# Optimization experiments

Hardware: AMD Instinct MI355X
Metric: run time of the kernel (lower is better)

## Reference

```python
import jax, jax.numpy as jnp
import numpy as np

N, E, M = 100000, 3200000, 1000000  # nodes, message edges, scored move edges
DIN, H = 128, 64


def setup_inputs() -> dict:
    key = jax.random.key(0)
    ks = jax.random.split(key, 20)
    rn = lambda k, shape, s=0.05: (jax.random.normal(k, shape, jnp.float32) * s)
    return {
        "x": jax.random.normal(ks[0], (N, DIN), jnp.float32),
        "edge_index": jax.random.randint(ks[1], (2, E), 0, N, jnp.int64),
        "move_edge_index": jax.random.randint(ks[2], (2, M), 0, N, jnp.int64),
        "lin1_w": rn(ks[3], (DIN, H)), "lin1_b": jnp.zeros((H,), jnp.float32),
        "lin2_w": rn(ks[4], (H, H)), "lin2_b": jnp.zeros((H,), jnp.float32),
        "conv1_wl": rn(ks[5], (H, H)), "conv1_bl": jnp.zeros((H,), jnp.float32),
        "conv1_wr": rn(ks[6], (H, H)),
        "conv2_wl": rn(ks[7], (H, H)), "conv2_bl": jnp.zeros((H,), jnp.float32),
        "conv2_wr": rn(ks[8], (H, H)),
        "mlp_w1": rn(ks[9], (2 * H, H)), "mlp_b1": jnp.zeros((H,), jnp.float32),
        "mlp_w2": rn(ks[10], (H, 1)), "mlp_b2": jnp.zeros((1,), jnp.float32),
    }


def reference(x, edge_index, move_edge_index,
              lin1_w, lin1_b, lin2_w, lin2_b,
              conv1_wl, conv1_bl, conv1_wr,
              conv2_wl, conv2_bl, conv2_wr,
              mlp_w1, mlp_b1, mlp_w2, mlp_b2):
    n = x.shape[0]
    src, dst = edge_index[0], edge_index[1]
    # mean-aggregation degrees (PyG SAGEConv default aggr='mean'; isolated nodes -> 0)
    deg = jax.ops.segment_sum(jnp.ones(src.shape, x.dtype), dst, num_segments=n)
    inv_deg = (jnp.where(deg > 0, 1.0 / jnp.maximum(deg, 1.0), 0.0))[:, None]

    def sage(h, wl, bl, wr):
        # out = W_l @ mean_j h_j + b_l + W_r @ h_i
        agg = jax.ops.segment_sum(h[src], dst, num_segments=n) * inv_deg
        return agg @ wl + bl + h @ wr

    h = jax.nn.relu(x @ lin1_w + lin1_b)
    h = jax.nn.relu(sage(h, conv1_wl, conv1_bl, conv1_wr))
    h = jax.nn.relu(h @ lin2_w + lin2_b)
    h = jax.nn.relu(sage(h, conv2_wl, conv2_bl, conv2_wr))

    # edge scoring: gather src/dst embeddings, concat, 2-layer MLP, tanh
    cat = jnp.concatenate([h[move_edge_index[0]], h[move_edge_index[1]]], axis=1)  # [M, 2H]
    logits = (jax.nn.relu(cat @ mlp_w1 + mlp_b1) @ mlp_w2 + mlp_b2).reshape(-1)
    return jnp.tanh(logits)
```

## Files before the change

### kernel.cpp

```cpp
#include <hip/hip_runtime.h>
#include <math.h>

#define MAXB 512
#define PART_BS 1024
#define NBLK_MAX 248
#define CAPB 96

typedef _Float16 f16;
typedef __attribute__((ext_vector_type(2))) _Float16 f16x2;
typedef __attribute__((ext_vector_type(4))) _Float16 f16x4;
typedef __attribute__((ext_vector_type(8))) _Float16 f16x8;
typedef __attribute__((ext_vector_type(4))) float f32x4;

static __device__ __forceinline__ unsigned short f2h(float f) {
    f16 h = (f16)f; return *(unsigned short*)&h;
}

__global__ __launch_bounds__(PART_BS) void k_part(const int* __restrict__ src,
                                                  const int* __restrict__ dst,
                                                  unsigned* __restrict__ bb,
                                                  int* __restrict__ cnt,
                                                  int E, int shift, int pcap,
                                                  int nblk, int nb) {
    __shared__ int h[MAXB];
    const int blk = blockIdx.x;
    const int b0 = blk * pcap;
    const int e1 = min(b0 + pcap, E);
    for (int i = threadIdx.x; i < MAXB; i += PART_BS) h[i] = 0;
    __syncthreads();
    const unsigned mask = (1u << shift) - 1u;
    for (int pos = b0 + (int)threadIdx.x * 8; pos < e1; pos += PART_BS * 8) {
        if (pos + 8 <= e1) {
            int4 d0 = *(const int4*)(dst + pos), d1 = *(const int4*)(dst + pos + 4);
            int4 s0 = *(const int4*)(src + pos), s1 = *(const int4*)(src + pos + 4);
            int dd[8] = {d0.x, d0.y, d0.z, d0.w, d1.x, d1.y, d1.z, d1.w};
            int ss[8] = {s0.x, s0.y, s0.z, s0.w, s1.x, s1.y, s1.z, s1.w};
#pragma unroll
            for (int k = 0; k < 8; ++k) {
                int b = dd[k] >> shift;
                int r = atomicAdd(&h[b], 1);
                if (r < CAPB)
                    bb[((size_t)b * nblk + blk) * CAPB + r] =
                        ((unsigned)ss[k] << shift) | ((unsigned)dd[k] & mask);
            }
        } else {
            for (int k = 0; pos + k < e1; ++k) {
                int d = dst[pos + k];
                int b = d >> shift;
                int r = atomicAdd(&h[b], 1);
                if (r < CAPB)
                    bb[((size_t)b * nblk + blk) * CAPB + r] =
                        ((unsigned)src[pos + k] << shift) | ((unsigned)d & mask);
            }
        }
    }
    __syncthreads();
    for (int i = threadIdx.x; i < nb; i += PART_BS)
        cnt[(size_t)i * nblk + blk] = min(h[i], CAPB);
}

__global__ __launch_bounds__(512) void k_bfill(const unsigned* __restrict__ bb,
                                               const int* __restrict__ cnt,
                                               int* __restrict__ row_st,
                                               int* __restrict__ row_en,
                                               float* __restrict__ inv_deg,
                                               int* __restrict__ csr,
                                               int N, int shift, int CAP, int nblk) {
    __shared__ int deg[512], cur[512], s[512];
    __shared__ int scnt[NBLK_MAX];
    int b = blockIdx.x;
    int t = threadIdx.x;
    int lo = b << shift;
    int hi = min(N, (b + 1) << shift);
    int nn = hi - lo;
    unsigned off = (unsigned)b * CAP;
    unsigned mask = (1u << shift) - 1u;
    const unsigned* seg = bb + (size_t)b * nblk * CAPB;

    for (int i = t; i < nblk; i += 512) scnt[i] = cnt[(size_t)b * nblk + i];
    deg[t] = 0;
    __syncthreads();
    const int tot = nblk * CAPB;
    for (int i = t; i < tot; i += 512) {
        int si = i / CAPB;
        int r = i - si * CAPB;
        if (r < scnt[si])
            atomicAdd(&deg[seg[i] & mask], 1);
    }
    __syncthreads();
    int d = deg[t];
    int pd = (d + 31) & ~31;
    s[t] = pd;
    __syncthreads();
    for (int o = 1; o < 512; o <<= 1) {
        int u = (t >= o) ? s[t - o] : 0;
        __syncthreads();
        s[t] += u;
        __syncthreads();
    }
    int excl = min(s[t] - pd, CAP);
    int pe = min(excl + pd, CAP);
    cur[t] = excl;
    if (t < nn) {
        row_st[lo + t] = (int)off + excl;
        row_en[lo + t] = (int)off + pe;
        inv_deg[lo + t] = d > 0 ? 1.0f / (float)d : 0.0f;
        for (int j = excl + d; j < pe; ++j) csr[off + j] = N;
    }
    __syncthreads();
    for (int i = t; i < tot; i += 512) {
        int si = i / CAPB;
        int r = i - si * CAPB;
        if (r < scnt[si]) {
            unsigned w = seg[i];
            int dl = (int)(w & mask);
            int pos = atomicAdd(&cur[dl], 1);
            if (pos < CAP) csr[off + pos] = (int)(w >> shift);
        }
    }
}

__global__ __launch_bounds__(256) void k_prep(
    const float* __restrict__ lin1_w, const float* __restrict__ c1_wl,
    const float* __restrict__ c1_wr, const float* __restrict__ lin2_w,
    const float* __restrict__ c2_wl, const float* __restrict__ c2_wr,
    const float* __restrict__ mlp_w1, const float* __restrict__ mlp_w2,
    unsigned short* __restrict__ Wt) {
    int i = blockIdx.x * 256 + threadIdx.x;
    for (; i < 36928; i += gridDim.x * 256) {
        float v;
        if (i < 8192)       { int j = i;         int n = j >> 7, k = j & 127; v = lin1_w[k * 64 + n]; }
        else if (i < 16384) { int j = i - 8192;  int n = j >> 7, k = j & 127;
                              v = (k < 64) ? c1_wl[k * 64 + n] : c1_wr[(k - 64) * 64 + n]; }
        else if (i < 20480) { int j = i - 16384; int n = j >> 6, k = j & 63;  v = lin2_w[k * 64 + n]; }
        else if (i < 28672) { int j = i - 20480; int n = j >> 7, k = j & 127;
                              v = (k < 64) ? c2_wl[k * 64 + n] : c2_wr[(k - 64) * 64 + n]; }
        else if (i < 32768) { int j = i - 28672; int n = j >> 6, k = j & 63;  v = mlp_w1[k * 64 + n]; }
        else if (i < 36864) { int j = i - 32768; int n = j >> 6, k = j & 63;  v = mlp_w1[(k + 64) * 64 + n]; }
        else                { v = mlp_w2[i - 36864]; }
        Wt[i] = f2h(v);
    }
}

__global__ __launch_bounds__(256) void k_gather_h(
    const _Float16* __restrict__ hh, const int* __restrict__ csr,
    const int* __restrict__ row_st, const int* __restrict__ row_en,
    const float* __restrict__ inv_deg, _Float16* __restrict__ out, int n) {
    int node = (blockIdx.x * 256 + (int)threadIdx.x) >> 6;
    if (node >= n) return;
    int lane = threadIdx.x & 63;
    int g = lane >> 3, sub = lane & 7;
    int base = row_st[node], end = row_en[node];
    float a[8] = {0.f, 0.f, 0.f, 0.f, 0.f, 0.f, 0.f, 0.f};
#if __has_builtin(__builtin_amdgcn_fdot2)
    const f16x2 one2 = {(f16)1.f, (f16)1.f};
#endif
    for (; base + 64 <= end; base += 64) {
        int4 sA = *(const int4*)&csr[base + 4 * g];
        int4 sB = *(const int4*)&csr[base + 32 + 4 * g];
        int sidx[8] = {sA.x, sA.y, sA.z, sA.w, sB.x, sB.y, sB.z, sB.w};
        f16x8 u[8];
#pragma unroll
        for (int t = 0; t < 8; ++t)
            u[t] = *(const f16x8*)(hh + (((unsigned)sidx[t] << 6) + ((unsigned)sub << 3)));
#if __has_builtin(__builtin_amdgcn_fdot2)
#pragma unroll
        for (int t = 0; t < 8; t += 2)
#pragma unroll
            for (int j = 0; j < 8; ++j) {
                f16x2 v = {u[t][j], u[t + 1][j]};
                a[j] = __builtin_amdgcn_fdot2(v, one2, a[j], false);
            }
#else
#pragma unroll
        for (int t = 0; t < 8; ++t)
#pragma unroll
            for (int j = 0; j < 8; ++j) a[j] += (float)u[t][j];
#endif
    }
    if (base < end) {
        int4 sA = *(const int4*)&csr[base + 4 * g];
        int sidx[4] = {sA.x, sA.y, sA.z, sA.w};
        f16x8 u[4];
#pragma unroll
        for (int t = 0; t < 4; ++t)
            u[t] = *(const f16x8*)(hh + (((unsigned)sidx[t] << 6) + ((unsigned)sub << 3)));
#if __has_builtin(__builtin_amdgcn_fdot2)
#pragma unroll
        for (int t = 0; t < 4; t += 2)
#pragma unroll
            for (int j = 0; j < 8; ++j) {
                f16x2 v = {u[t][j], u[t + 1][j]};
                a[j] = __builtin_amdgcn_fdot2(v, one2, a[j], false);
            }
#else
#pragma unroll
        for (int t = 0; t < 4; ++t)
#pragma unroll
            for (int j = 0; j < 8; ++j) a[j] += (float)u[t][j];
#endif
    }
#pragma unroll
    for (int j = 0; j < 8; ++j) {
        a[j] += __shfl_xor(a[j], 8, 64);
        a[j] += __shfl_xor(a[j], 16, 64);
        a[j] += __shfl_xor(a[j], 32, 64);
    }
    if (g == 0) {
        float idv = inv_deg[node];
        f16x8 o;
#pragma unroll
        for (int j = 0; j < 8; ++j) o[j] = (f16)(a[j] * idv);
        *(f16x8*)(out + (((unsigned)node << 6) + ((unsigned)sub << 3))) = o;
    }
}

__global__ __launch_bounds__(256) void k_mm1(
    const float* __restrict__ x, const unsigned short* __restrict__ Wtg,
    const float* __restrict__ bias, unsigned short* __restrict__ outh, int n) {
    __shared__ alignas(16) unsigned short sW[64 * 136];
    const int tid = threadIdx.x;
    const int row0 = blockIdx.x * 64;
    if (blockIdx.x == 0 && tid < 8)
        ((uint4*)(outh + (size_t)n * 64))[tid] = (uint4){0, 0, 0, 0};
    for (int i = tid; i < 64 * 16; i += 256) {
        int nn = i >> 4, c = i & 15;
        *(uint4*)&sW[(nn * 17 + c) * 8] = *(const uint4*)&Wtg[i * 8];
    }
    __syncthreads();
    const int lane = tid & 63, w = tid >> 6;
    const int m = lane & 15, q = lane >> 4;
    const int gr = min(row0 + 16 * w + m, n - 1);
    const float* ar = x + (size_t)gr * 128;
    f32x4 acc[4];
#pragma unroll
    for (int c = 0; c < 4; ++c) acc[c] = (f32x4){0.f, 0.f, 0.f, 0.f};
#pragma unroll
    for (int kk = 0; kk < 4; ++kk) {
        float4 a0 = *(const float4*)(ar + kk * 32 + q * 8);
        float4 a1 = *(const float4*)(ar + kk * 32 + q * 8 + 4);
        f16x8 af;
        af[0] = (f16)a0.x; af[1] = (f16)a0.y; af[2] = (f16)a0.z; af[3] = (f16)a0.w;
        af[4] = (f16)a1.x; af[5] = (f16)a1.y; af[6] = (f16)a1.z; af[7] = (f16)a1.w;
#pragma unroll
        for (int c = 0; c < 4; ++c) {
            f16x8 bf = *(const f16x8*)&sW[((16 * c + m) * 17 + (kk * 4 + q)) * 8];
            acc[c] = __builtin_amdgcn_mfma_f32_16x16x32_f16(af, bf, acc[c], 0, 0, 0);
        }
    }
#pragma unroll
    for (int c = 0; c < 4; ++c) {
        int col = 16 * c + m;
        float bv = bias[col];
#pragma unroll
        for (int i = 0; i < 4; ++i) {
            int r = row0 + 16 * w + q * 4 + i;
            if (r < n) outh[(size_t)r * 64 + col] = f2h(fmaxf(acc[c][i] + bv, 0.f));
        }
    }
}

__global__ __launch_bounds__(256) void k_mm23(
    const unsigned short* __restrict__ aggH, const unsigned short* __restrict__ h1,
    const unsigned short* __restrict__ Wcg, const float* __restrict__ bl,
    const unsigned short* __restrict__ Wl2g, const float* __restrict__ b2,
    unsigned short* __restrict__ outh, int n) {
    __shared__ alignas(16) unsigned short sm[64 * 72 + 64 * 136];
    unsigned short* hA = sm;
    unsigned short* sW = sm + 64 * 72;
    const int tid = threadIdx.x;
    const int row0 = blockIdx.x * 64;
    for (int i = tid; i < 64 * 16; i += 256) {
        int nn = i >> 4, c = i & 15;
        *(uint4*)&sW[(nn * 17 + c) * 8] = *(const uint4*)&Wcg[i * 8];
    }
    __syncthreads();
    const int lane = tid & 63, w = tid >> 6;
    const int m = lane & 15, q = lane >> 4;
    const int gr = min(row0 + 16 * w + m, n - 1);
    f32x4 acc[4];
#pragma unroll
    for (int c = 0; c < 4; ++c) acc[c] = (f32x4){0.f, 0.f, 0.f, 0.f};
#pragma unroll
    for (int kk = 0; kk < 4; ++kk) {
        const unsigned short* ap = (kk < 2)
            ? (aggH + (size_t)gr * 64 + kk * 32 + q * 8)
            : (h1 + (size_t)gr * 64 + (kk - 2) * 32 + q * 8);
        f16x8 af = *(const f16x8*)ap;
#pragma unroll
        for (int c = 0; c < 4; ++c) {
            f16x8 bf = *(const f16x8*)&sW[((16 * c + m) * 17 + (kk * 4 + q)) * 8];
            acc[c] = __builtin_amdgcn_mfma_f32_16x16x32_f16(af, bf, acc[c], 0, 0, 0);
        }
    }
#pragma unroll
    for (int c = 0; c < 4; ++c) {
        int col = 16 * c + m;
        float bv = bl[col];
#pragma unroll
        for (int i = 0; i < 4; ++i)
            hA[(16 * w + q * 4 + i) * 72 + col] = f2h(fmaxf(acc[c][i] + bv, 0.f));
    }
    __syncthreads();
    for (int i = tid; i < 64 * 8; i += 256) {
        int nn = i >> 3, c = i & 7;
        *(uint4*)&sW[(nn * 9 + c) * 8] = *(const uint4*)&Wl2g[i * 8];
    }
    __syncthreads();
    f32x4 acc2[4];
#pragma unroll
    for (int c = 0; c < 4; ++c) acc2[c] = (f32x4){0.f, 0.f, 0.f, 0.f};
#pragma unroll
    for (int kk = 0; kk < 2; ++kk) {
        f16x8 af = *(const f16x8*)&hA[(16 * w + m) * 72 + kk * 32 + q * 8];
#pragma unroll
        for (int c = 0; c < 4; ++c) {
            f16x8 bf = *(const f16x8*)&sW[((16 * c + m) * 9 + (kk * 4 + q)) * 8];
            acc2[c] = __builtin_amdgcn_mfma_f32_16x16x32_f16(af, bf, acc2[c], 0, 0, 0);
        }
    }
#pragma unroll
    for (int c = 0; c < 4; ++c) {
        int col = 16 * c + m;
        float bv = b2[col];
#pragma unroll
        for (int i = 0; i < 4; ++i) {
            int r = row0 + 16 * w + q * 4 + i;
            if (r < n) outh[(size_t)r * 64 + col] = f2h(fmaxf(acc2[c][i] + bv, 0.f));
        }
    }
}

__global__ __launch_bounds__(256) void k_mm456(
    const unsigned short* __restrict__ aggH, const unsigned short* __restrict__ h3,
    const unsigned short* __restrict__ Wcg, const float* __restrict__ bl,
    const unsigned short* __restrict__ Wpg, const unsigned short* __restrict__ Wqg,
    const float* __restrict__ b1, unsigned short* __restrict__ Ph,
    unsigned short* __restrict__ Qh, int n) {
    __shared__ alignas(16) unsigned short sm[64 * 72 + 2 * 64 * 72];
    unsigned short* hA = sm;
    unsigned short* sW = sm + 64 * 72;
    const int tid = threadIdx.x;
    const int row0 = blockIdx.x * 64;
    for (int i = tid; i < 64 * 16; i += 256) {
        int nn = i >> 4, c = i & 15;
        *(uint4*)&sW[(nn * 17 + c) * 8] = *(const uint4*)&Wcg[i * 8];
    }
    __syncthreads();
    const int lane = tid & 63, w = tid >> 6;
    const int m = lane & 15, q = lane >> 4;
    const int gr = min(row0 + 16 * w + m, n - 1);
    f32x4 acc[4];
#pragma unroll
    for (int c = 0; c < 4; ++c) acc[c] = (f32x4){0.f, 0.f, 0.f, 0.f};
#pragma unroll
    for (int kk = 0; kk < 4; ++kk) {
        const unsigned short* ap = (kk < 2)
            ? (aggH + (size_t)gr * 64 + kk * 32 + q * 8)
            : (h3 + (size_t)gr * 64 + (kk - 2) * 32 + q * 8);
        f16x8 af = *(const f16x8*)ap;
#pragma unroll
        for (int c = 0; c < 4; ++c) {
            f16x8 bf = *(const f16x8*)&sW[((16 * c + m) * 17 + (kk * 4 + q)) * 8];
            acc[c] = __builtin_amdgcn_mfma_f32_16x16x32_f16(af, bf, acc[c], 0, 0, 0);
        }
    }
#pragma unroll
    for (int c = 0; c < 4; ++c) {
        int col = 16 * c + m;
        float bv = bl[col];
#pragma unroll
        for (int i = 0; i < 4; ++i)
            hA[(16 * w + q * 4 + i) * 72 + col] = f2h(fmaxf(acc[c][i] + bv, 0.f));
    }
    __syncthreads();
    for (int i = tid; i < 64 * 8; i += 256) {
        int nn = i >> 3, c = i & 7;
        *(uint4*)&sW[(nn * 9 + c) * 8] = *(const uint4*)&Wpg[i * 8];
        *(uint4*)&sW[4608 + (nn * 9 + c) * 8] = *(const uint4*)&Wqg[i * 8];
    }
    __syncthreads();
    f32x4 accP[4], accQ[4];
#pragma unroll
    for (int c = 0; c < 4; ++c) {
        accP[c] = (f32x4){0.f, 0.f, 0.f, 0.f};
        accQ[c] = (f32x4){0.f, 0.f, 0.f, 0.f};
    }
#pragma unroll
    for (int kk = 0; kk < 2; ++kk) {
        f16x8 af = *(const f16x8*)&hA[(16 * w + m) * 72 + kk * 32 + q * 8];
#pragma unroll
        for (int c = 0; c < 4; ++c) {
            f16x8 bp = *(const f16x8*)&sW[((16 * c + m) * 9 + (kk * 4 + q)) * 8];
            f16x8 bq = *(const f16x8*)&sW[4608 + ((16 * c + m) * 9 + (kk * 4 + q)) * 8];
            accP[c] = __builtin_amdgcn_mfma_f32_16x16x32_f16(af, bp, accP[c], 0, 0, 0);
            accQ[c] = __builtin_amdgcn_mfma_f32_16x16x32_f16(af, bq, accQ[c], 0, 0, 0);
        }
    }
#pragma unroll
    for (int c = 0; c < 4; ++c) {
        int col = 16 * c + m;
        float bv = b1[col];
#pragma unroll
        for (int i = 0; i < 4; ++i) {
            int r = row0 + 16 * w + q * 4 + i;
            if (r < n) {
                Ph[(size_t)r * 64 + col] = f2h(accP[c][i] + bv);
                Qh[(size_t)r * 64 + col] = f2h(accQ[c][i]);
            }
        }
    }
}

__global__ __launch_bounds__(256) void k_score_h(
    const _Float16* __restrict__ P, const _Float16* __restrict__ Q,
    const int* __restrict__ msrc, const int* __restrict__ mdst,
    const _Float16* __restrict__ w2h, const float* __restrict__ b2,
    float* __restrict__ out, int M) {
    int gid = blockIdx.x * 256 + threadIdx.x;
    int e = gid >> 3;
    if (e >= M) return;
    int l = gid & 7;
    int s = msrc[e], d = mdst[e];
    f16x8 p = *(const f16x8*)(P + (((unsigned)s << 6) + ((unsigned)l << 3)));
    f16x8 q = *(const f16x8*)(Q + (((unsigned)d << 6) + ((unsigned)l << 3)));
    f16x8 w = *(const f16x8*)(w2h + ((unsigned)l << 3));
    f16x8 u = p + q;
    f16x8 z = {(f16)0, (f16)0, (f16)0, (f16)0, (f16)0, (f16)0, (f16)0, (f16)0};
    u = __builtin_elementwise_max(u, z);
    float partial;
#if __has_builtin(__builtin_amdgcn_fdot2)
    f16x2 u01 = {u[0], u[1]}, u23 = {u[2], u[3]}, u45 = {u[4], u[5]}, u67 = {u[6], u[7]};
    f16x2 w01 = {w[0], w[1]}, w23 = {w[2], w[3]}, w45 = {w[4], w[5]}, w67 = {w[6], w[7]};
    partial = __builtin_amdgcn_fdot2(u01, w01,
              __builtin_amdgcn_fdot2(u23, w23,
              __builtin_amdgcn_fdot2(u45, w45,
              __builtin_amdgcn_fdot2(u67, w67, 0.f, false), false), false), false);
#else
    partial = 0.f;
#pragma unroll
    for (int i = 0; i < 8; ++i) partial += (float)u[i] * (float)w[i];
#endif
    partial += __shfl_xor(partial, 1, 8);
    partial += __shfl_xor(partial, 2, 8);
    partial += __shfl_xor(partial, 4, 8);
    if (l == 0) {
        float xx = partial + b2[0];
        float t = __expf(2.f * xx);
        out[e] = (t - 1.f) / (t + 1.f);
    }
}

extern "C" void kernel_launch(void* const* d_in, const int* in_sizes, int n_in,
                              void* d_out, int out_size, void* d_ws, size_t ws_size,
                              hipStream_t stream) {
    const float* x      = (const float*)d_in[0];
    const int*   ei     = (const int*)d_in[1];
    const int*   mei    = (const int*)d_in[2];
    const float* lin1_w = (const float*)d_in[3];
    const float* lin1_b = (const float*)d_in[4];
    const float* lin2_w = (const float*)d_in[5];
    const float* lin2_b = (const float*)d_in[6];
    const float* c1_wl  = (const float*)d_in[7];
    const float* c1_bl  = (const float*)d_in[8];
    const float* c1_wr  = (const float*)d_in[9];
    const float* c2_wl  = (const float*)d_in[10];
    const float* c2_bl  = (const float*)d_in[11];
    const float* c2_wr  = (const float*)d_in[12];
    const float* mlp_w1 = (const float*)d_in[13];
    const float* mlp_b1 = (const float*)d_in[14];
    const float* mlp_w2 = (const float*)d_in[15];
    const float* mlp_b2 = (const float*)d_in[16];

    const int N = in_sizes[0] / 128;
    const int E = in_sizes[1] / 2;
    const int M = in_sizes[2] / 2;
    const int* src  = ei;
    const int* dstE = ei + E;
    const int* msrc = mei;
    const int* mdst = mei + M;

    int shift = 8;
    while ((((N - 1) >> shift) + 1) > MAXB) ++shift;
    const int nbuckets = ((N - 1) >> shift) + 1;
    long long avg = (((long long)E << shift) / N) + 1;
    int CAP = (int)((2 * avg + 2047) & ~1023LL);

    const size_t N64 = (size_t)N * 64;
    const size_t aliasBytes = (3 * N64 + 64) * 2;
    int nblk = NBLK_MAX;
    while (nblk > 1 && (size_t)nblk * nbuckets * CAPB * 4 > aliasBytes) --nblk;
    int pcap = (((E + nblk - 1) / nblk) + 7) & ~7;
    nblk = (E + pcap - 1) / pcap;

    unsigned short* Hh   = (unsigned short*)d_ws;
    unsigned short* aggH = Hh + N64 + 64;
    unsigned short* Qh   = aggH + N64;
    float* inv_deg = (float*)(Qh + N64);
    int*   row_st  = (int*)(inv_deg + N);
    int*   row_en  = row_st + N;
    int*   cnt     = row_en + N;
    unsigned short* Wt = (unsigned short*)(cnt + (size_t)nbuckets * NBLK_MAX);
    int*   csr     = (int*)(Wt + 36928 + 32);
    unsigned* bb   = (unsigned*)Hh;
    float* outf = (float*)d_out;

    const int nbN = (N + 63) / 64;
    const int nbM = (int)(((long long)M * 8 + 255) / 256);
    const int nbG = (int)(((long long)N * 64 + 255) / 256);

    k_prep<<<64, 256, 0, stream>>>(lin1_w, c1_wl, c1_wr, lin2_w, c2_wl, c2_wr,
                                   mlp_w1, mlp_w2, Wt);
    k_part<<<nblk, PART_BS, 0, stream>>>(src, dstE, bb, cnt, E, shift, pcap,
                                         nblk, nbuckets);
    k_bfill<<<nbuckets, 512, 0, stream>>>(bb, cnt, row_st, row_en,
                                          inv_deg, csr, N, shift, CAP, nblk);

    k_mm1<<<nbN, 256, 0, stream>>>(x, Wt + 0, lin1_b, Hh, N);

    k_gather_h<<<nbG, 256, 0, stream>>>((const _Float16*)Hh, csr, row_st, row_en,
                                        inv_deg, (_Float16*)aggH, N);
    k_mm23<<<nbN, 256, 0, stream>>>(aggH, Hh, Wt + 8192, c1_bl,
                                    Wt + 16384, lin2_b, Hh, N);

    k_gather_h<<<nbG, 256, 0, stream>>>((const _Float16*)Hh, csr, row_st, row_en,
                                        inv_deg, (_Float16*)aggH, N);
    k_mm456<<<nbN, 256, 0, stream>>>(aggH, Hh, Wt + 20480, c2_bl,
                                     Wt + 28672, Wt + 32768, mlp_b1,
                                     Hh, Qh, N);

    k_score_h<<<nbM, 256, 0, stream>>>((const _Float16*)Hh, (const _Float16*)Qh,
                                       msrc, mdst, (const _Float16*)(Wt + 36864),
                                       mlp_b2, outf, M);
}
```

Measured before the change: 386.7 us.

## Compute degrees with global atomics and build compact CSR via global scan

Node degrees are now counted with global atomics during the partition pass, and a new per-256-node kernel pads them, scans them, and reserves contiguous ranges with an atomic counter, replacing the fixed per-bucket CAP region. The bucket fill kernel then only scatters sources into the precomputed row offsets, which removes its degree pass and block-wide scan. In exchange it adds 3.2M global atomics, a memset and an extra launch. Row ranges are no longer ordered by node, which may hurt locality in the later gathers.

```diff
diff --git a/kernel.cpp b/kernel.cpp
--- a/kernel.cpp
+++ b/kernel.cpp
@@ -16,12 +16,13 @@
     f16 h = (f16)f; return *(unsigned short*)&h;
 }
 
-__global__ __launch_bounds__(PART_BS) void k_part(const int* __restrict__ src,
-                                                  const int* __restrict__ dst,
-                                                  unsigned* __restrict__ bb,
-                                                  int* __restrict__ cnt,
-                                                  int E, int shift, int pcap,
-                                                  int nblk, int nb) {
+__global__ __launch_bounds__(PART_BS) void k_part2(const int* __restrict__ src,
+                                                   const int* __restrict__ dst,
+                                                   unsigned* __restrict__ bb,
+                                                   int* __restrict__ cnt,
+                                                   int* __restrict__ deg,
+                                                   int E, int shift, int pcap,
+                                                   int nblk, int nb) {
     __shared__ int h[MAXB];
     const int blk = blockIdx.x;
     const int b0 = blk * pcap;
@@ -38,6 +39,7 @@
 #pragma unroll
             for (int k = 0; k < 8; ++k) {
                 int b = dd[k] >> shift;
+                atomicAdd(&deg[dd[k]], 1);
                 int r = atomicAdd(&h[b], 1);
                 if (r < CAPB)
                     bb[((size_t)b * nblk + blk) * CAPB + r] =
@@ -47,6 +49,7 @@
             for (int k = 0; pos + k < e1; ++k) {
                 int d = dst[pos + k];
                 int b = d >> shift;
+                atomicAdd(&deg[d], 1);
                 int r = atomicAdd(&h[b], 1);
                 if (r < CAPB)
                     bb[((size_t)b * nblk + blk) * CAPB + r] =
@@ -59,63 +62,64 @@
         cnt[(size_t)i * nblk + blk] = min(h[i], CAPB);
 }
 
-__global__ __launch_bounds__(512) void k_bfill(const unsigned* __restrict__ bb,
-                                               const int* __restrict__ cnt,
-                                               int* __restrict__ row_st,
-                                               int* __restrict__ row_en,
-                                               float* __restrict__ inv_deg,
-                                               int* __restrict__ csr,
-                                               int N, int shift, int CAP, int nblk) {
-    __shared__ int deg[512], cur[512], s[512];
+__global__ __launch_bounds__(256) void k_rows(const int* __restrict__ deg,
+                                              int* __restrict__ gtot,
+                                              int* __restrict__ row_st,
+                                              int* __restrict__ row_en,
+                                              float* __restrict__ inv_deg,
+                                              int* __restrict__ csr, int N) {
+    __shared__ int s[256];
+    __shared__ int basesh;
+    int t = threadIdx.x;
+    int node = blockIdx.x * 256 + t;
+    int d = (node < N) ? deg[node] : 0;
+    int pd = (d + 31) & ~31;
+    s[t] = pd;
+    __syncthreads();
+    for (int o = 1; o < 256; o <<= 1) {
+        int u = (t >= o) ? s[t - o] : 0;
+        __syncthreads();
+        s[t] += u;
+        __syncthreads();
+    }
+    if (t == 255) basesh = atomicAdd(gtot, s[255]);
+    __syncthreads();
+    int excl = basesh + s[t] - pd;
+    if (node < N) {
+        row_st[node] = excl;
+        row_en[node] = excl + pd;
+        inv_deg[node] = d > 0 ? 1.0f / (float)d : 0.0f;
+        for (int j = d; j < pd; ++j) csr[excl + j] = N;
+    }
+}
+
+__global__ __launch_bounds__(512) void k_bfill2(const unsigned* __restrict__ bb,
+                                                const int* __restrict__ cnt,
+                                                const int* __restrict__ row_st,
+                                                int* __restrict__ csr,
+                                                int N, int shift, int nblk) {
+    __shared__ int curL[512];
     __shared__ int scnt[NBLK_MAX];
     int b = blockIdx.x;
     int t = threadIdx.x;
     int lo = b << shift;
     int hi = min(N, (b + 1) << shift);
     int nn = hi - lo;
-    unsigned off = (unsigned)b * CAP;
     unsigned mask = (1u << shift) - 1u;
     const unsigned* seg = bb + (size_t)b * nblk * CAPB;
 
     for (int i = t; i < nblk; i += 512) scnt[i] = cnt[(size_t)b * nblk + i];
-    deg[t] = 0;
+    if (t < nn) curL[t] = row_st[lo + t];
     __syncthreads();
     const int tot = nblk * CAPB;
-    for (int i = t; i < tot; i += 512) {
-        int si = i / CAPB;
-        int r = i - si * CAPB;
-        if (r < scnt[si])
-            atomicAdd(&deg[seg[i] & mask], 1);
-    }
-    __syncthreads();
-    int d = deg[t];
-    int pd = (d + 31) & ~31;
-    s[t] = pd;
-    __syncthreads();
-    for (int o = 1; o < 512; o <<= 1) {
-        int u = (t >= o) ? s[t - o] : 0;
-        __syncthreads();
-        s[t] += u;
-        __syncthreads();
-    }
-    int excl = min(s[t] - pd, CAP);
-    int pe = min(excl + pd, CAP);
-    cur[t] = excl;
-    if (t < nn) {
-        row_st[lo + t] = (int)off + excl;
-        row_en[lo + t] = (int)off + pe;
-        inv_deg[lo + t] = d > 0 ? 1.0f / (float)d : 0.0f;
-        for (int j = excl + d; j < pe; ++j) csr[off + j] = N;
-    }
-    __syncthreads();
     for (int i = t; i < tot; i += 512) {
         int si = i / CAPB;
         int r = i - si * CAPB;
         if (r < scnt[si]) {
             unsigned w = seg[i];
             int dl = (int)(w & mask);
-            int pos = atomicAdd(&cur[dl], 1);
-            if (pos < CAP) csr[off + pos] = (int)(w >> shift);
+            int pos = atomicAdd(&curL[dl], 1);
+            csr[pos] = (int)(w >> shift);
         }
     }
 }
@@ -483,8 +487,6 @@
     int shift = 8;
     while ((((N - 1) >> shift) + 1) > MAXB) ++shift;
     const int nbuckets = ((N - 1) >> shift) + 1;
-    long long avg = (((long long)E << shift) / N) + 1;
-    int CAP = (int)((2 * avg + 2047) & ~1023LL);
 
     const size_t N64 = (size_t)N * 64;
     const size_t aliasBytes = (3 * N64 + 64) * 2;
@@ -499,7 +501,8 @@
     float* inv_deg = (float*)(Qh + N64);
     int*   row_st  = (int*)(inv_deg + N);
     int*   row_en  = row_st + N;
-    int*   cnt     = row_en + N;
+    int*   deg     = row_en + N;
+    int*   cnt     = deg + N + 8;
     unsigned short* Wt = (unsigned short*)(cnt + (size_t)nbuckets * NBLK_MAX);
     int*   csr     = (int*)(Wt + 36928 + 32);
     unsigned* bb   = (unsigned*)Hh;
@@ -508,13 +511,16 @@
     const int nbN = (N + 63) / 64;
     const int nbM = (int)(((long long)M * 8 + 255) / 256);
     const int nbG = (int)(((long long)N * 64 + 255) / 256);
-
+    const int nbR = (N + 255) / 256;
+
+    hipMemsetAsync(deg, 0, (size_t)(N + 1) * sizeof(int), stream);
     k_prep<<<64, 256, 0, stream>>>(lin1_w, c1_wl, c1_wr, lin2_w, c2_wl, c2_wr,
                                    mlp_w1, mlp_w2, Wt);
-    k_part<<<nblk, PART_BS, 0, stream>>>(src, dstE, bb, cnt, E, shift, pcap,
-                                         nblk, nbuckets);
-    k_bfill<<<nbuckets, 512, 0, stream>>>(bb, cnt, row_st, row_en,
-                                          inv_deg, csr, N, shift, CAP, nblk);
+    k_part2<<<nblk, PART_BS, 0, stream>>>(src, dstE, bb, cnt, deg, E, shift,
+                                          pcap, nblk, nbuckets);
+    k_rows<<<nbR, 256, 0, stream>>>(deg, deg + N, row_st, row_en,
+                                    inv_deg, csr, N);
+    k_bfill2<<<nbuckets, 512, 0, stream>>>(bb, cnt, row_st, csr, N, shift, nblk);
 
     k_mm1<<<nbN, 256, 0, stream>>>(x, Wt + 0, lin1_b, Hh, N);
 
```

Measured after the change: 496.4 us. +28.4%, slower.
